# Performance work log

Hardware: AMD Instinct MI355X
Metric: run time of the kernel (lower is better)

## Reference

```python
import jax, jax.numpy as jnp
import numpy as np

HIDDEN = 1024
HEADS = 16
HEAD_DIM = HIDDEN // HEADS
GAMMA = 0.5
B, S = 2, 2048


def setup_inputs() -> dict:
    key = jax.random.key(0)
    ks = jax.random.split(key, 9)
    sc = 1.0 / np.sqrt(HIDDEN)
    x = jax.random.normal(ks[0], (B, S, HIDDEN), dtype=jnp.float32)
    attn_mask = jnp.zeros((S, S), dtype=bool)  # True = masked; all-False here
    Wq = jax.random.normal(ks[1], (HIDDEN, HIDDEN), dtype=jnp.float32) * sc
    bq = jnp.zeros((HIDDEN,), dtype=jnp.float32)
    Wk = jax.random.normal(ks[2], (HIDDEN, HIDDEN), dtype=jnp.float32) * sc
    bk = jnp.zeros((HIDDEN,), dtype=jnp.float32)
    Wv = jax.random.normal(ks[3], (HIDDEN, HIDDEN), dtype=jnp.float32) * sc
    bv = jnp.zeros((HIDDEN,), dtype=jnp.float32)
    Wo = jax.random.normal(ks[4], (HIDDEN, HIDDEN), dtype=jnp.float32) * sc
    bo = jnp.zeros((HIDDEN,), dtype=jnp.float32)
    return {"x": x, "attn_mask": attn_mask, "Wq": Wq, "bq": bq,
            "Wk": Wk, "bk": bk, "Wv": Wv, "bv": bv, "Wo": Wo, "bo": bo}


def reference(x, attn_mask, Wq, bq, Wk, bk, Wv, bv, Wo, bo):
    Bn, Sn, _ = x.shape
    # projections (torch Linear: x @ W.T + b), reshape to [B, H, S, Dh]
    def proj(W, b):
        y = x @ W.T + b
        return y.reshape(Bn, Sn, HEADS, HEAD_DIM).transpose(0, 2, 1, 3)
    q, k, v = proj(Wq, bq), proj(Wk, bk), proj(Wv, bv)
    scores = jnp.einsum('bhqd,bhkd->bhqk', q, k) / np.sqrt(HEAD_DIM)
    # diversity bias: cosine similarity of raw x (F.normalize eps=1e-12)
    normed = x / jnp.maximum(jnp.linalg.norm(x, axis=-1, keepdims=True), 1e-12)
    sim = jnp.einsum('bqd,bkd->bqk', normed, normed)
    scores = scores - GAMMA * sim[:, None, :, :]
    scores = jnp.where(attn_mask[None, None, :, :], -jnp.inf, scores)
    probs = jax.nn.softmax(scores, axis=-1)
    ctx = jnp.einsum('bhqk,bhkd->bhqd', probs, v)
    ctx = ctx.transpose(0, 2, 1, 3).reshape(Bn, Sn, HIDDEN)
    return ctx @ Wo.T + bo
```

## Files before the change

### kernel.cpp

```cpp
#include <hip/hip_runtime.h>

#define HID 1024
#define SEQ 2048
#define NB 2
#define NH 16
#define HD 64

#define C1 0.1803368801111204f
#define C2 0.7213475204444817f

typedef __attribute__((ext_vector_type(8))) short bf16x8;
typedef __attribute__((ext_vector_type(8))) unsigned short u16x8;
typedef __attribute__((ext_vector_type(4))) float f32x4;

__device__ __forceinline__ unsigned short f2bf(float f) {
  unsigned u = __builtin_bit_cast(unsigned, f);
  u += 0x7fffu + ((u >> 16) & 1u);
  return (unsigned short)(u >> 16);
}
__device__ __forceinline__ float bf2f(unsigned short u) {
  return __builtin_bit_cast(float, ((unsigned)u) << 16);
}

#define GLOAD16(gsrc, ldst)                                                     \
  __builtin_amdgcn_global_load_lds(                                             \
      (const __attribute__((address_space(1))) void*)(gsrc),                    \
      (__attribute__((address_space(3))) void*)(ldst), 16, 0, 0)

__global__ __launch_bounds__(256) void prep_kernel(
    const float* __restrict__ x,
    const float* __restrict__ Wq, const float* __restrict__ Wk,
    const float* __restrict__ Wv, const float* __restrict__ Wo,
    unsigned short* __restrict__ Wb,
    unsigned short* __restrict__ xb, unsigned short* __restrict__ nxb) {
  int tid = threadIdx.x;
  if (blockIdx.x < 2048) {
    int i = blockIdx.x * 256 + tid;
    const int per = (HID * HID) / 8;
    int m = i / per;
    const float* sp = (m == 0) ? Wq : (m == 1) ? Wk : (m == 2) ? Wv : Wo;
    int j = (i - m * per) * 8;
    const float4* p = reinterpret_cast<const float4*>(sp + j);
    float4 a = p[0], b = p[1];
    u16x8 o;
    o[0] = f2bf(a.x); o[1] = f2bf(a.y); o[2] = f2bf(a.z); o[3] = f2bf(a.w);
    o[4] = f2bf(b.x); o[5] = f2bf(b.y); o[6] = f2bf(b.z); o[7] = f2bf(b.w);
    *reinterpret_cast<u16x8*>(Wb + (size_t)i * 8) = o;
  } else {
    int row = blockIdx.x - 2048;
    const float4 v = reinterpret_cast<const float4*>(x + (size_t)row * HID)[tid];
    float ss = v.x * v.x + v.y * v.y + v.z * v.z + v.w * v.w;
#pragma unroll
    for (int off = 32; off; off >>= 1) ss += __shfl_xor(ss, off, 64);
    __shared__ float wsum[4];
    if ((tid & 63) == 0) wsum[tid >> 6] = ss;
    __syncthreads();
    float tot = wsum[0] + wsum[1] + wsum[2] + wsum[3];
    float inv = 1.0f / fmaxf(sqrtf(tot), 1e-12f);
    ushort4 a, b;
    a.x = f2bf(v.x); a.y = f2bf(v.y); a.z = f2bf(v.z); a.w = f2bf(v.w);
    b.x = f2bf(v.x * inv); b.y = f2bf(v.y * inv);
    b.z = f2bf(v.z * inv); b.w = f2bf(v.w * inv);
    reinterpret_cast<ushort4*>(xb  + (size_t)row * HID)[tid] = a;
    reinterpret_cast<ushort4*>(nxb + (size_t)row * HID)[tid] = b;
  }
}

#define ISSUE_TILE(kk, bf)                                                      \
  do {                                                                          \
    GLOAD16(Ab + (kk) * 32, &As[bf][lw]);                                       \
    GLOAD16(Ab + 16 * K + (kk) * 32, &As[bf][lw + 512]);                        \
    GLOAD16(Bb + (kk) * 32, &Bs[bf][lw]);                                       \
    GLOAD16(Bb + 16 * K + (kk) * 32, &Bs[bf][lw + 512]);                        \
  } while (0)

#define GEMM_K_LOOP                                                             \
  ISSUE_TILE(0, 0);                                                             \
  ISSUE_TILE(1, 1);                                                             \
  int buf = 0;                                                                  \
  for (int kk = 0; kk < 32; ++kk) {                                             \
    if (kk + 2 < 32) {                                                          \
      int nb = buf == 0 ? 2 : buf - 1;                                          \
      ISSUE_TILE(kk + 2, nb);                                                   \
    }                                                                           \
    if (kk < 30)       asm volatile("s_waitcnt vmcnt(8)" ::: "memory");         \
    else if (kk == 30) asm volatile("s_waitcnt vmcnt(4)" ::: "memory");         \
    else               asm volatile("s_waitcnt vmcnt(0)" ::: "memory");         \
    __builtin_amdgcn_s_barrier();                                               \
    const unsigned short* Ar = &As[buf][0];                                     \
    const unsigned short* Br = &Bs[buf][0];                                     \
    bf16x8 af[4], bfr[4];                                                       \
    _Pragma("unroll")                                                           \
    for (int i = 0; i < 4; i++) {                                               \
      af[i]  = *reinterpret_cast<const bf16x8*>(&Ar[(wr * 64 + i * 16 + lr) * 32 + g * 8]); \
      bfr[i] = *reinterpret_cast<const bf16x8*>(&Br[(wc * 64 + i * 16 + lr) * 32 + g * 8]); \
    }                                                                           \
    _Pragma("unroll")                                                           \
    for (int i = 0; i < 4; i++)                                                 \
      _Pragma("unroll")                                                         \
      for (int j = 0; j < 4; j++)                                               \
        acc[i][j] = __builtin_amdgcn_mfma_f32_16x16x32_bf16(af[i], bfr[j], acc[i][j], 0, 0, 0); \
    __builtin_amdgcn_sched_barrier(0);                                          \
    asm volatile("s_waitcnt lgkmcnt(0)" ::: "memory");                          \
    __builtin_amdgcn_s_barrier();                                               \
    buf = buf == 2 ? 0 : buf + 1;                                               \
  }

__global__ __launch_bounds__(256) void mega_gemm(
    const unsigned short* __restrict__ xb, const unsigned short* __restrict__ nxb,
    const unsigned short* __restrict__ Wb,
    unsigned short* __restrict__ QK, unsigned short* __restrict__ VT,
    unsigned short* __restrict__ D2,
    const float* __restrict__ bq, const float* __restrict__ bk,
    const float* __restrict__ bv, const unsigned char* __restrict__ mask) {
  const int K = HID;
  int bid = (blockIdx.x & 7) * 130 + (blockIdx.x >> 3);
  int mode, m0, n0;
  const unsigned short *A, *B;
  size_t zoff = 0;
  if (bid < 512) {
    mode = 0; n0 = (bid >> 5) * 128; m0 = (bid & 31) * 128;
    A = xb; B = Wb;
  } else if (bid < 768) {
    mode = 3; int t = bid - 512; m0 = (t >> 5) * 128; n0 = (t & 31) * 128;
    A = Wb + (size_t)2 * HID * HID; B = xb;
  } else {
    mode = 1; int t = bid - 768; int z = 0;
    if (t >= 136) { z = 1; t -= 136; }
    int a = (int)((sqrtf(8.0f * t + 1.0f) - 1.0f) * 0.5f);
    while (a * (a + 1) / 2 > t) a--;
    while ((a + 1) * (a + 2) / 2 <= t) a++;
    int bI = t - a * (a + 1) / 2;
    m0 = bI * 128; n0 = a * 128;
    A = nxb + (size_t)z * SEQ * HID; B = A;
    zoff = (size_t)z * SEQ * SEQ;
  }

  __shared__ __align__(16) unsigned short As[3][128 * 32];
  __shared__ __align__(16) unsigned short Bs[3][128 * 32];
  int tid = threadIdx.x, lane = tid & 63, wid = tid >> 6;
  int g = lane >> 4, lr = lane & 15;
  int wr = wid >> 1, wc = wid & 1;
  const unsigned short* Ab = A + (size_t)(m0 + wid * 32 + (lane >> 2)) * K + (lane & 3) * 8;
  const unsigned short* Bb = B + (size_t)(n0 + wid * 32 + (lane >> 2)) * K + (lane & 3) * 8;
  const int lw = wid * 1024;

  f32x4 acc[4][4] = {};
  GEMM_K_LOOP

#pragma unroll
  for (int i = 0; i < 4; i++)
#pragma unroll
    for (int j = 0; j < 4; j++) {
      int col = n0 + wc * 64 + j * 16 + lr;
#pragma unroll
      for (int r = 0; r < 4; r++) {
        int row = m0 + wr * 64 + i * 16 + 4 * g + r;
        float v = acc[i][j][r];
        if (mode == 0) {
          const float* bp = (col < 1024) ? bq : bk;
          QK[(size_t)row * 2048 + col] = f2bf(v + bp[col & 1023]);
        } else if (mode == 3) {
          VT[(size_t)row * 4096 + col] = f2bf(v + bv[row]);
        } else {
          float t1 = -C2 * v + (mask[(size_t)row * SEQ + col] ? -1e30f : 0.0f);
          D2[zoff + (size_t)row * SEQ + col] = f2bf(t1);
          if (m0 != n0) {
            float t2 = -C2 * v + (mask[(size_t)col * SEQ + row] ? -1e30f : 0.0f);
            D2[zoff + (size_t)col * SEQ + row] = f2bf(t2);
          }
        }
      }
    }
}

__global__ __launch_bounds__(256) void gemm_out(
    const unsigned short* __restrict__ A, const unsigned short* __restrict__ B,
    float* __restrict__ C, const float* __restrict__ b0) {
  const int K = HID;
  __shared__ __align__(16) unsigned short As[3][128 * 32];
  __shared__ __align__(16) unsigned short Bs[3][128 * 32];
  int tid = threadIdx.x, lane = tid & 63, wid = tid >> 6;
  int g = lane >> 4, lr = lane & 15;
  int wr = wid >> 1, wc = wid & 1;
  int bid = (blockIdx.x & 7) * 32 + (blockIdx.x >> 3);
  int n0 = (bid >> 5) * 128, m0 = (bid & 31) * 128;
  const unsigned short* Ab = A + (size_t)(m0 + wid * 32 + (lane >> 2)) * K + (lane & 3) * 8;
  const unsigned short* Bb = B + (size_t)(n0 + wid * 32 + (lane >> 2)) * K + (lane & 3) * 8;
  const int lw = wid * 1024;

  f32x4 acc[4][4] = {};
  GEMM_K_LOOP

#pragma unroll
  for (int i = 0; i < 4; i++)
#pragma unroll
    for (int j = 0; j < 4; j++) {
      int col = n0 + wc * 64 + j * 16 + lr;
#pragma unroll
      for (int r = 0; r < 4; r++) {
        int row = m0 + wr * 64 + i * 16 + 4 * g + r;
        C[(size_t)row * HID + col] = acc[i][j][r] + b0[col];
      }
    }
}

__global__ __launch_bounds__(256, 4) void flash_kernel(
    const unsigned short* __restrict__ QK,
    const unsigned short* __restrict__ VT,
    const unsigned short* __restrict__ D2,
    unsigned short* __restrict__ ctxb) {
  int h = blockIdx.x, qt = blockIdx.y, b = blockIdx.z;
  int tid = threadIdx.x, wid = tid >> 6, lane = tid & 63;
  int g = lane >> 4, lr = lane & 15;
  __shared__ __align__(16) unsigned short Ks[2][64 * 64];
  __shared__ __align__(16) unsigned short Vt[2][64 * 64];
  const size_t ld = 2 * HID;
  const size_t bS = (size_t)b * SEQ;
  const int qbase = qt * 64 + wid * 16;

  const unsigned short* qp = QK + (bS + qbase + lr) * ld + h * HD + g * 8;
  bf16x8 qf0 = *reinterpret_cast<const bf16x8*>(qp);
  bf16x8 qf1 = *reinterpret_cast<const bf16x8*>(qp + 32);

  const int p0 = wid * 16 + (lane >> 3);
  const int key0 = ((p0 >> 5) & 1) * 32 + (((p0 >> 2) & 3) << 3)
                 + ((p0 >> 4) & 1) * 4 + (p0 & 3);
  const unsigned short* gK0 = QK + (bS + key0) * ld + HID + h * HD
                              + (((lane & 7) ^ (lane >> 3)) << 3);
  const unsigned short* gK1 = gK0 + 16 * ld;

  const unsigned short* gV0 = VT + (size_t)(h * HD + wid * 16 + (lane >> 3)) * (2 * SEQ)
                              + bS + (((lane & 7) ^ (lane >> 3)) << 3);
  const unsigned short* gV1 = gV0 + (size_t)8 * (2 * SEQ);

  const unsigned short* bD = D2 + (size_t)b * SEQ * SEQ
                             + (size_t)(qbase + lr) * SEQ + 8 * g;

  GLOAD16(gK0, &Ks[0][wid * 1024]);
  GLOAD16(gK1, &Ks[0][wid * 1024 + 512]);
  GLOAD16(gV0, &Vt[0][wid * 1024]);
  GLOAD16(gV1, &Vt[0][wid * 1024 + 512]);
  ushort4 bvc[4];
  bvc[0] = *reinterpret_cast<const ushort4*>(bD + 0);
  bvc[1] = *reinterpret_cast<const ushort4*>(bD + 4);
  bvc[2] = *reinterpret_cast<const ushort4*>(bD + 32);
  bvc[3] = *reinterpret_cast<const ushort4*>(bD + 36);
  __syncthreads();

  f32x4 acc[4] = {};
  f32x4 rsacc = {};
  const int kb0 = lr * 64 + ((g ^ (lr & 7)) << 3);
  bf16x8 ones;
#pragma unroll
  for (int i = 0; i < 8; i++) ones[i] = 0x3F80;

  for (int kt = 0; kt < 32; ++kt) {
    const int cb = kt & 1;
    const unsigned short* ks = &Ks[cb][0];
    const unsigned short* vt = &Vt[cb][0];
    ushort4 bvn[4];
    if (kt < 31) {
      GLOAD16(gK0 + (size_t)(kt + 1) * 64 * ld, &Ks[cb ^ 1][wid * 1024]);
      GLOAD16(gK1 + (size_t)(kt + 1) * 64 * ld, &Ks[cb ^ 1][wid * 1024 + 512]);
      GLOAD16(gV0 + (kt + 1) * 64, &Vt[cb ^ 1][wid * 1024]);
      GLOAD16(gV1 + (kt + 1) * 64, &Vt[cb ^ 1][wid * 1024 + 512]);
      const unsigned short* bn = bD + (kt + 1) * 64;
      bvn[0] = *reinterpret_cast<const ushort4*>(bn + 0);
      bvn[1] = *reinterpret_cast<const ushort4*>(bn + 4);
      bvn[2] = *reinterpret_cast<const ushort4*>(bn + 32);
      bvn[3] = *reinterpret_cast<const ushort4*>(bn + 36);
    }

    f32x4 s[4];
    __builtin_amdgcn_s_setprio(1);
#pragma unroll
    for (int kc = 0; kc < 4; kc++) {
      bf16x8 kf0 = *reinterpret_cast<const bf16x8*>(ks + kc * 1024 + kb0);
      bf16x8 kf1 = *reinterpret_cast<const bf16x8*>(ks + kc * 1024 + (kb0 ^ 32));
      f32x4 z = {};
      z = __builtin_amdgcn_mfma_f32_16x16x32_bf16(kf0, qf0, z, 0, 0, 0);
      s[kc] = __builtin_amdgcn_mfma_f32_16x16x32_bf16(kf1, qf1, z, 0, 0, 0);
    }
    __builtin_amdgcn_s_setprio(0);

    bf16x8 pa[2];
#pragma unroll
    for (int c2 = 0; c2 < 2; c2++) {
      float p0f = exp2f(fmaf(s[2 * c2][0], C1, bf2f(bvc[2 * c2].x)));
      float p1f = exp2f(fmaf(s[2 * c2][1], C1, bf2f(bvc[2 * c2].y)));
      float p2f = exp2f(fmaf(s[2 * c2][2], C1, bf2f(bvc[2 * c2].z)));
      float p3f = exp2f(fmaf(s[2 * c2][3], C1, bf2f(bvc[2 * c2].w)));
      float p4f = exp2f(fmaf(s[2 * c2 + 1][0], C1, bf2f(bvc[2 * c2 + 1].x)));
      float p5f = exp2f(fmaf(s[2 * c2 + 1][1], C1, bf2f(bvc[2 * c2 + 1].y)));
      float p6f = exp2f(fmaf(s[2 * c2 + 1][2], C1, bf2f(bvc[2 * c2 + 1].z)));
      float p7f = exp2f(fmaf(s[2 * c2 + 1][3], C1, bf2f(bvc[2 * c2 + 1].w)));
      uint4 W;
      W.x = __builtin_amdgcn_perm(__builtin_bit_cast(unsigned, p1f),
                                  __builtin_bit_cast(unsigned, p0f), 0x07060302u);
      W.y = __builtin_amdgcn_perm(__builtin_bit_cast(unsigned, p3f),
                                  __builtin_bit_cast(unsigned, p2f), 0x07060302u);
      W.z = __builtin_amdgcn_perm(__builtin_bit_cast(unsigned, p5f),
                                  __builtin_bit_cast(unsigned, p4f), 0x07060302u);
      W.w = __builtin_amdgcn_perm(__builtin_bit_cast(unsigned, p7f),
                                  __builtin_bit_cast(unsigned, p6f), 0x07060302u);
      pa[c2] = __builtin_bit_cast(bf16x8, W);
    }

    __builtin_amdgcn_s_setprio(1);
#pragma unroll
    for (int c2 = 0; c2 < 2; c2++) {
      rsacc = __builtin_amdgcn_mfma_f32_16x16x32_bf16(pa[c2], ones, rsacc, 0, 0, 0);
#pragma unroll
      for (int df = 0; df < 4; df++) {
        bf16x8 vf = *reinterpret_cast<const bf16x8*>(
            vt + (df * 16 + lr) * 64 + (((4 * c2 + g) ^ (lr & 7)) << 3));
        acc[df] = __builtin_amdgcn_mfma_f32_16x16x32_bf16(pa[c2], vf, acc[df], 0, 0, 0);
      }
    }
    __builtin_amdgcn_s_setprio(0);

    if (kt < 31) {
      bvc[0] = bvn[0]; bvc[1] = bvn[1]; bvc[2] = bvn[2]; bvc[3] = bvn[3];
    }
    __syncthreads();
  }
  float l0 = 1.0f / rsacc[0], l1 = 1.0f / rsacc[1];
  float l2 = 1.0f / rsacc[2], l3 = 1.0f / rsacc[3];
  unsigned short* op = ctxb + (bS + qbase + 4 * g) * HID + h * HD + lr;
#pragma unroll
  for (int df = 0; df < 4; df++) {
    op[0 * HID + df * 16] = f2bf(acc[df][0] * l0);
    op[1 * HID + df * 16] = f2bf(acc[df][1] * l1);
    op[2 * HID + df * 16] = f2bf(acc[df][2] * l2);
    op[3 * HID + df * 16] = f2bf(acc[df][3] * l3);
  }
}

extern "C" void kernel_launch(void* const* d_in, const int* in_sizes, int n_in,
                              void* d_out, int out_size, void* d_ws, size_t ws_size,
                              hipStream_t stream) {
  const float* x = (const float*)d_in[0];
  const unsigned char* mask = (const unsigned char*)d_in[1];
  const float* Wq = (const float*)d_in[2];
  const float* bq = (const float*)d_in[3];
  const float* Wk = (const float*)d_in[4];
  const float* bk = (const float*)d_in[5];
  const float* Wv = (const float*)d_in[6];
  const float* bv = (const float*)d_in[7];
  const float* Wo = (const float*)d_in[8];
  const float* bo = (const float*)d_in[9];
  float* out = (float*)d_out;

  char* ws = (char*)d_ws;
  const size_t MiB = 1024 * 1024;
  unsigned short* xb  = (unsigned short*)(ws + 0 * MiB);
  unsigned short* nxb = (unsigned short*)(ws + 8 * MiB);
  unsigned short* Wb  = (unsigned short*)(ws + 16 * MiB);
  unsigned short* QK  = (unsigned short*)(ws + 24 * MiB);
  unsigned short* VT  = (unsigned short*)(ws + 40 * MiB);
  unsigned short* D2  = (unsigned short*)(ws + 48 * MiB);
  unsigned short* ctx = (unsigned short*)(ws + 64 * MiB);

  prep_kernel<<<6144, 256, 0, stream>>>(x, Wq, Wk, Wv, Wo, Wb, xb, nxb);
  mega_gemm<<<1040, 256, 0, stream>>>(xb, nxb, Wb, QK, VT, D2, bq, bk, bv, mask);
  flash_kernel<<<dim3(NH, SEQ / 64, NB), 256, 0, stream>>>(QK, VT, D2, ctx);
  gemm_out<<<256, 256, 0, stream>>>(
      ctx, Wb + (size_t)3 * HID * HID, out, bo);
}
```

Baseline: 238.4 us.

## Use single-buffered BK=64 swizzled GEMM loop, simpler block mapping, raw v_exp

Replaces the triple-buffered BK=32 GEMM main loop with a single-buffered BK=64 loop that uses an XOR-swizzled LDS layout and plain __syncthreads, in both mega_gemm and gemm_out. It also drops the XCD-aware block index remapping in favour of a direct row-major tile mapping (gemm_out gets a 2D grid), and swaps exp2f for the raw v_exp_f32 instruction in the flash kernel. The swizzle targets LDS bank conflicts, and the larger K step halves the number of barriers per tile. In exchange, loads are no longer overlapped with MFMA work, and the new block mapping may lose L2 locality across XCDs.

New measurement: 204.7 us. 1.16x faster.

```diff
diff --git a/kernel.cpp b/kernel.cpp
--- a/kernel.cpp
+++ b/kernel.cpp
@@ -20,6 +20,11 @@
 }
 __device__ __forceinline__ float bf2f(unsigned short u) {
   return __builtin_bit_cast(float, ((unsigned)u) << 16);
+}
+__device__ __forceinline__ float fexp2(float x) {
+  float r;
+  asm("v_exp_f32 %0, %1" : "=v"(r) : "v"(x));
+  return r;
 }
 
 #define GLOAD16(gsrc, ldst)                                                     \
@@ -66,44 +71,31 @@
   }
 }
 
-#define ISSUE_TILE(kk, bf)                                                      \
-  do {                                                                          \
-    GLOAD16(Ab + (kk) * 32, &As[bf][lw]);                                       \
-    GLOAD16(Ab + 16 * K + (kk) * 32, &As[bf][lw + 512]);                        \
-    GLOAD16(Bb + (kk) * 32, &Bs[bf][lw]);                                       \
-    GLOAD16(Bb + 16 * K + (kk) * 32, &Bs[bf][lw + 512]);                        \
-  } while (0)
-
-#define GEMM_K_LOOP                                                             \
-  ISSUE_TILE(0, 0);                                                             \
-  ISSUE_TILE(1, 1);                                                             \
-  int buf = 0;                                                                  \
-  for (int kk = 0; kk < 32; ++kk) {                                             \
-    if (kk + 2 < 32) {                                                          \
-      int nb = buf == 0 ? 2 : buf - 1;                                          \
-      ISSUE_TILE(kk + 2, nb);                                                   \
+#define GEMM_K_LOOP64                                                           \
+  for (int kt = 0; kt < 16; ++kt) {                                             \
+    _Pragma("unroll")                                                           \
+    for (int j = 0; j < 4; j++) {                                               \
+      GLOAD16(Ab + (size_t)j * 32 * K + kt * 64, &As[j * 2048 + wid * 512]);    \
+      GLOAD16(Bb + (size_t)j * 32 * K + kt * 64, &Bs[j * 2048 + wid * 512]);    \
     }                                                                           \
-    if (kk < 30)       asm volatile("s_waitcnt vmcnt(8)" ::: "memory");         \
-    else if (kk == 30) asm volatile("s_waitcnt vmcnt(4)" ::: "memory");         \
-    else               asm volatile("s_waitcnt vmcnt(0)" ::: "memory");         \
-    __builtin_amdgcn_s_barrier();                                               \
-    const unsigned short* Ar = &As[buf][0];                                     \
-    const unsigned short* Br = &Bs[buf][0];                                     \
-    bf16x8 af[4], bfr[4];                                                       \
+    __syncthreads();                                                            \
     _Pragma("unroll")                                                           \
-    for (int i = 0; i < 4; i++) {                                               \
-      af[i]  = *reinterpret_cast<const bf16x8*>(&Ar[(wr * 64 + i * 16 + lr) * 32 + g * 8]); \
-      bfr[i] = *reinterpret_cast<const bf16x8*>(&Br[(wc * 64 + i * 16 + lr) * 32 + g * 8]); \
+    for (int h = 0; h < 2; h++) {                                               \
+      bf16x8 af[4], bfr[4];                                                     \
+      _Pragma("unroll")                                                         \
+      for (int i = 0; i < 4; i++) {                                             \
+        af[i]  = *reinterpret_cast<const bf16x8*>(                              \
+            &As[(wr * 64 + i * 16 + lr) * 64 + ((((h << 2) + g) ^ (lr & 7)) << 3)]); \
+        bfr[i] = *reinterpret_cast<const bf16x8*>(                              \
+            &Bs[(wc * 64 + i * 16 + lr) * 64 + ((((h << 2) + g) ^ (lr & 7)) << 3)]); \
+      }                                                                         \
+      _Pragma("unroll")                                                         \
+      for (int i = 0; i < 4; i++)                                               \
+        _Pragma("unroll")                                                       \
+        for (int j = 0; j < 4; j++)                                             \
+          acc[i][j] = __builtin_amdgcn_mfma_f32_16x16x32_bf16(af[i], bfr[j], acc[i][j], 0, 0, 0); \
     }                                                                           \
-    _Pragma("unroll")                                                           \
-    for (int i = 0; i < 4; i++)                                                 \
-      _Pragma("unroll")                                                         \
-      for (int j = 0; j < 4; j++)                                               \
-        acc[i][j] = __builtin_amdgcn_mfma_f32_16x16x32_bf16(af[i], bfr[j], acc[i][j], 0, 0, 0); \
-    __builtin_amdgcn_sched_barrier(0);                                          \
-    asm volatile("s_waitcnt lgkmcnt(0)" ::: "memory");                          \
-    __builtin_amdgcn_s_barrier();                                               \
-    buf = buf == 2 ? 0 : buf + 1;                                               \
+    __syncthreads();                                                            \
   }
 
 __global__ __launch_bounds__(256) void mega_gemm(
@@ -114,12 +106,12 @@
     const float* __restrict__ bq, const float* __restrict__ bk,
     const float* __restrict__ bv, const unsigned char* __restrict__ mask) {
   const int K = HID;
-  int bid = (blockIdx.x & 7) * 130 + (blockIdx.x >> 3);
+  int bid = blockIdx.x;
   int mode, m0, n0;
   const unsigned short *A, *B;
   size_t zoff = 0;
   if (bid < 512) {
-    mode = 0; n0 = (bid >> 5) * 128; m0 = (bid & 31) * 128;
+    mode = 0; m0 = (bid >> 4) * 128; n0 = (bid & 15) * 128;
     A = xb; B = Wb;
   } else if (bid < 768) {
     mode = 3; int t = bid - 512; m0 = (t >> 5) * 128; n0 = (t & 31) * 128;
@@ -136,17 +128,18 @@
     zoff = (size_t)z * SEQ * SEQ;
   }
 
-  __shared__ __align__(16) unsigned short As[3][128 * 32];
-  __shared__ __align__(16) unsigned short Bs[3][128 * 32];
+  __shared__ __align__(16) unsigned short As[128 * 64];
+  __shared__ __align__(16) unsigned short Bs[128 * 64];
   int tid = threadIdx.x, lane = tid & 63, wid = tid >> 6;
   int g = lane >> 4, lr = lane & 15;
   int wr = wid >> 1, wc = wid & 1;
-  const unsigned short* Ab = A + (size_t)(m0 + wid * 32 + (lane >> 2)) * K + (lane & 3) * 8;
-  const unsigned short* Bb = B + (size_t)(n0 + wid * 32 + (lane >> 2)) * K + (lane & 3) * 8;
-  const int lw = wid * 1024;
+  const unsigned short* Ab = A + (size_t)(m0 + wid * 8 + (lane >> 3)) * K
+                             + (((lane & 7) ^ (lane >> 3)) << 3);
+  const unsigned short* Bb = B + (size_t)(n0 + wid * 8 + (lane >> 3)) * K
+                             + (((lane & 7) ^ (lane >> 3)) << 3);
 
   f32x4 acc[4][4] = {};
-  GEMM_K_LOOP
+  GEMM_K_LOOP64
 
 #pragma unroll
   for (int i = 0; i < 4; i++)
@@ -178,19 +171,19 @@
     const unsigned short* __restrict__ A, const unsigned short* __restrict__ B,
     float* __restrict__ C, const float* __restrict__ b0) {
   const int K = HID;
-  __shared__ __align__(16) unsigned short As[3][128 * 32];
-  __shared__ __align__(16) unsigned short Bs[3][128 * 32];
+  __shared__ __align__(16) unsigned short As[128 * 64];
+  __shared__ __align__(16) unsigned short Bs[128 * 64];
   int tid = threadIdx.x, lane = tid & 63, wid = tid >> 6;
   int g = lane >> 4, lr = lane & 15;
   int wr = wid >> 1, wc = wid & 1;
-  int bid = (blockIdx.x & 7) * 32 + (blockIdx.x >> 3);
-  int n0 = (bid >> 5) * 128, m0 = (bid & 31) * 128;
-  const unsigned short* Ab = A + (size_t)(m0 + wid * 32 + (lane >> 2)) * K + (lane & 3) * 8;
-  const unsigned short* Bb = B + (size_t)(n0 + wid * 32 + (lane >> 2)) * K + (lane & 3) * 8;
-  const int lw = wid * 1024;
+  int m0 = blockIdx.y * 128, n0 = blockIdx.x * 128;
+  const unsigned short* Ab = A + (size_t)(m0 + wid * 8 + (lane >> 3)) * K
+                             + (((lane & 7) ^ (lane >> 3)) << 3);
+  const unsigned short* Bb = B + (size_t)(n0 + wid * 8 + (lane >> 3)) * K
+                             + (((lane & 7) ^ (lane >> 3)) << 3);
 
   f32x4 acc[4][4] = {};
-  GEMM_K_LOOP
+  GEMM_K_LOOP64
 
 #pragma unroll
   for (int i = 0; i < 4; i++)
@@ -287,14 +280,14 @@
     bf16x8 pa[2];
 #pragma unroll
     for (int c2 = 0; c2 < 2; c2++) {
-      float p0f = exp2f(fmaf(s[2 * c2][0], C1, bf2f(bvc[2 * c2].x)));
-      float p1f = exp2f(fmaf(s[2 * c2][1], C1, bf2f(bvc[2 * c2].y)));
-      float p2f = exp2f(fmaf(s[2 * c2][2], C1, bf2f(bvc[2 * c2].z)));
-      float p3f = exp2f(fmaf(s[2 * c2][3], C1, bf2f(bvc[2 * c2].w)));
-      float p4f = exp2f(fmaf(s[2 * c2 + 1][0], C1, bf2f(bvc[2 * c2 + 1].x)));
-      float p5f = exp2f(fmaf(s[2 * c2 + 1][1], C1, bf2f(bvc[2 * c2 + 1].y)));
-      float p6f = exp2f(fmaf(s[2 * c2 + 1][2], C1, bf2f(bvc[2 * c2 + 1].z)));
-      float p7f = exp2f(fmaf(s[2 * c2 + 1][3], C1, bf2f(bvc[2 * c2 + 1].w)));
+      float p0f = fexp2(fmaf(s[2 * c2][0], C1, bf2f(bvc[2 * c2].x)));
+      float p1f = fexp2(fmaf(s[2 * c2][1], C1, bf2f(bvc[2 * c2].y)));
+      float p2f = fexp2(fmaf(s[2 * c2][2], C1, bf2f(bvc[2 * c2].z)));
+      float p3f = fexp2(fmaf(s[2 * c2][3], C1, bf2f(bvc[2 * c2].w)));
+      float p4f = fexp2(fmaf(s[2 * c2 + 1][0], C1, bf2f(bvc[2 * c2 + 1].x)));
+      float p5f = fexp2(fmaf(s[2 * c2 + 1][1], C1, bf2f(bvc[2 * c2 + 1].y)));
+      float p6f = fexp2(fmaf(s[2 * c2 + 1][2], C1, bf2f(bvc[2 * c2 + 1].z)));
+      float p7f = fexp2(fmaf(s[2 * c2 + 1][3], C1, bf2f(bvc[2 * c2 + 1].w)));
       uint4 W;
       W.x = __builtin_amdgcn_perm(__builtin_bit_cast(unsigned, p1f),
                                   __builtin_bit_cast(unsigned, p0f), 0x07060302u);
@@ -365,6 +358,6 @@
   prep_kernel<<<6144, 256, 0, stream>>>(x, Wq, Wk, Wv, Wo, Wb, xb, nxb);
   mega_gemm<<<1040, 256, 0, stream>>>(xb, nxb, Wb, QK, VT, D2, bq, bk, bv, mask);
   flash_kernel<<<dim3(NH, SEQ / 64, NB), 256, 0, stream>>>(QK, VT, D2, ctx);
-  gemm_out<<<256, 256, 0, stream>>>(
+  gemm_out<<<dim3(8, 32), 256, 0, stream>>>(
       ctx, Wb + (size_t)3 * HID * HID, out, bo);
 }
```
